# Optimization experiments

Hardware: AMD Instinct MI355X
Metric: run time of the kernel (lower is better)

Reference implementation:

```python
import jax, jax.numpy as jnp
import numpy as np


def dct_matrices(N):
    # torch_dct-style unnormalized DCT-II (norm=None): X_k = 2 * sum_n x_n cos(pi*(2n+1)k/(2N))
    n = jnp.arange(N, dtype=jnp.float32)
    ang = jnp.pi * (2.0 * n[None, :] + 1.0) * n[:, None] / (2.0 * N)  # [k, n]
    D = 2.0 * jnp.cos(ang)                                            # forward DCT matrix [k, n]
    w = jnp.where(n == 0, 0.5, 1.0)                                   # half-weight on DC term
    M = (jnp.cos(ang).T * w[None, :]) / (2.0 * N)                     # inverse DCT matrix [n, k]
    return D, M


def setup_inputs() -> dict:
    key = jax.random.key(0)
    k1, k2, k3 = jax.random.split(key, 3)
    B, c_in, c_out, H, W, kh, kw = 8, 64, 128, 128, 128, 5, 5
    K = float(np.sqrt(1.0 / (c_in * kh * kw)))
    x = jax.random.normal(k1, (B, c_in, H, W), dtype=jnp.float32)
    weight = (2.0 * jax.random.uniform(k2, (c_out, c_in, kh, kw), dtype=jnp.float32) - 1.0) * K
    bias = (2.0 * jax.random.uniform(k3, (c_out,), dtype=jnp.float32) - 1.0) * K
    return {"x": x, "weight": weight, "bias": bias}


def reference(x, weight, bias):
    B, c_in, H, W = x.shape
    c_out, _, kh, kw = weight.shape
    D, M = dct_matrices(H)

    # DCT-II along H axis of input
    xd = jnp.einsum('kh,bchw->bckw', D, x)            # (B, c_in, H, W)
    xf = jnp.fft.rfft(xd, axis=-1)                    # (B, c_in, H, Wf) complex

    # Pad kernel along H to full size, DCT along H, rFFT along W with n=W
    wpad = jnp.pad(weight, ((0, 0), (0, 0), (0, H - kh), (0, 0)))
    wd = jnp.einsum('kh,oihw->oikw', D, wpad)         # (c_out, c_in, H, kw)
    wf = jnp.fft.rfft(wd, n=W, axis=-1)               # (c_out, c_in, H, Wf) complex

    # Broadcast complex multiply + reduce over c_in (fused via einsum)
    hf = jnp.einsum('bchw,ochw->bohw', xf, wf)        # (B, c_out, H, Wf)
    h = jnp.fft.irfft(hf, n=W, axis=-1)               # (B, c_out, H, W)

    # Inverse DCT along H, add bias, stride slice (stride = 1)
    h = jnp.einsum('nk,bokw->bonw', M, h) + bias[None, :, None, None]
    return h[:, :, ::1, ::1]
```

## Files before the change

### kernel.cpp

```cpp
#include <hip/hip_runtime.h>


using half8v = __attribute__((ext_vector_type(8))) _Float16;
using half4v = __attribute__((ext_vector_type(4))) _Float16;
using f32x4  = __attribute__((ext_vector_type(4))) float;

#define PI_F 3.14159265358979323846f

__device__ __forceinline__ int sw_off(int n, int k, int K, int mask) {
    int c = k >> 3;
    return n * K + (((c ^ (n & mask)) << 3) | (k & 7));
}

__global__ void k_dm(_Float16* __restrict__ D, _Float16* __restrict__ M) {
    int k = blockIdx.x;
    int h = threadIdx.x;
    float ang = PI_F * (float)((2 * h + 1) * k) * (1.0f / 256.0f);
    float c = cosf(ang);
    D[k * 128 + h] = (_Float16)(2.0f * c);
    float wk = (k == 0) ? 0.5f : 1.0f;
    M[h * 128 + k] = (_Float16)(c * wk * (1.0f / 256.0f));
}

__global__ void k_wd(const float* __restrict__ w, _Float16* __restrict__ WD) {
    int bid = blockIdx.x;
    int kf = bid / 10, s = bid % 10;
    int j = s >> 1, ci0 = (s & 1) << 5;
    float dv[5];
#pragma unroll
    for (int i = 0; i < 5; ++i)
        dv[i] = 2.0f * cosf(PI_F * (float)((2 * i + 1) * kf) * (1.0f / 256.0f));
    for (int e = threadIdx.x; e < 4096; e += 256) {
        int co = e >> 5, t = e & 31, ci = ci0 + t;
        const float* wp = w + (co * 64 + ci) * 25 + j;
        float acc = 0.f;
#pragma unroll
        for (int i = 0; i < 5; ++i) acc += dv[i] * wp[i * 5];
        WD[bid * 4096 + e] = (_Float16)acc;
    }
}

__device__ __forceinline__ void gemm128(const _Float16* lA, const _Float16* lB,
                                        f32x4 acc[4][4], int tid) {
    int lane = tid & 63, ln = lane & 15, q = lane >> 4;
    int wave = tid >> 6, wm = wave >> 1, wn = wave & 1;
#pragma unroll
    for (int s = 0; s < 4; ++s) {
        half8v af[4], bf[4];
#pragma unroll
        for (int mt = 0; mt < 4; ++mt) {
            int m = wm * 64 + mt * 16 + ln;
            af[mt] = *(const half8v*)(&lA[m * 128 + (((s * 4 + q) ^ (m & 15)) << 3)]);
        }
#pragma unroll
        for (int nt = 0; nt < 4; ++nt) {
            int n = wn * 64 + nt * 16 + ln;
            bf[nt] = *(const half8v*)(&lB[n * 128 + (((s * 4 + q) ^ (n & 15)) << 3)]);
        }
#pragma unroll
        for (int mt = 0; mt < 4; ++mt)
#pragma unroll
            for (int nt = 0; nt < 4; ++nt)
                acc[mt][nt] = __builtin_amdgcn_mfma_f32_16x16x32_f16(af[mt], bf[nt], acc[mt][nt], 0, 0, 0);
    }
}

__device__ __forceinline__ void stage_copyA(const _Float16* __restrict__ g, _Float16* l, int tid) {
    const half8v* gs = (const half8v*)g;
#pragma unroll
    for (int r = 0; r < 8; ++r) {
        int gg = tid + r * 256;
        int m = gg >> 4, c = gg & 15;
        *(half8v*)(&l[m * 128 + (((c ^ (m & 15)) << 3))]) = gs[gg];
    }
}

__device__ __forceinline__ void stage_transB(const _Float16* __restrict__ src, int row_stride,
                                             _Float16* l, int K, int mask, int nblocks, int tid) {
    for (int blk = tid; blk < nblocks; blk += 256) {
        int kb = blk >> 4, wb = blk & 15;
        int k0 = kb * 4, w0 = wb * 8;
        half8v r0 = *(const half8v*)(&src[(k0 + 0) * row_stride + w0]);
        half8v r1 = *(const half8v*)(&src[(k0 + 1) * row_stride + w0]);
        half8v r2 = *(const half8v*)(&src[(k0 + 2) * row_stride + w0]);
        half8v r3 = *(const half8v*)(&src[(k0 + 3) * row_stride + w0]);
#pragma unroll
        for (int dw = 0; dw < 8; ++dw) {
            int n = w0 + dw;
            half4v p = {r0[dw], r1[dw], r2[dw], r3[dw]};
            *(half4v*)(&l[sw_off(n, k0, K, mask)]) = p;
        }
    }
}

__global__ __launch_bounds__(256) void k_dctH(const float* __restrict__ x,
                                              const _Float16* __restrict__ Dg,
                                              _Float16* __restrict__ xd) {
    __shared__ _Float16 lA[128 * 128];
    __shared__ _Float16 lB[128 * 128];
    int b = blockIdx.x >> 6, ci = blockIdx.x & 63;
    int tid = threadIdx.x;

    stage_copyA(Dg, lA, tid);

    const float* xs = x + (long)(b * 64 + ci) * 16384;
#pragma unroll
    for (int rep = 0; rep < 2; ++rep) {
        int blk = tid + rep * 256;
        int hb = blk >> 4, wb = blk & 15;
        int h0 = hb * 4, w0 = wb * 8;
        f32x4 f[4][2];
#pragma unroll
        for (int dh = 0; dh < 4; ++dh) {
            f[dh][0] = *(const f32x4*)(&xs[(h0 + dh) * 128 + w0]);
            f[dh][1] = *(const f32x4*)(&xs[(h0 + dh) * 128 + w0 + 4]);
        }
#pragma unroll
        for (int dw = 0; dw < 8; ++dw) {
            int n = w0 + dw;
            half4v p = {(_Float16)f[0][dw >> 2][dw & 3], (_Float16)f[1][dw >> 2][dw & 3],
                        (_Float16)f[2][dw >> 2][dw & 3], (_Float16)f[3][dw >> 2][dw & 3]};
            *(half4v*)(&lB[sw_off(n, h0, 128, 15)]) = p;
        }
    }
    __syncthreads();

    f32x4 acc[4][4] = {};
    gemm128(lA, lB, acc, tid);

    int lane = tid & 63, ln = lane & 15, q = lane >> 4;
    int wave = tid >> 6, wm = wave >> 1, wn = wave & 1;
#pragma unroll
    for (int mt = 0; mt < 4; ++mt)
#pragma unroll
        for (int nt = 0; nt < 4; ++nt)
#pragma unroll
            for (int r = 0; r < 4; ++r) {
                int kk = wm * 64 + mt * 16 + q * 4 + r;
                int wcol = wn * 64 + nt * 16 + ln;
                xd[((long)(kk * 8 + b) * 64 + ci) * 128 + wcol] = (_Float16)acc[mt][nt][r];
            }
}

__global__ __launch_bounds__(256) void k_conv(const _Float16* __restrict__ xd,
                                              const _Float16* __restrict__ WD,
                                              _Float16* __restrict__ y2) {
    __shared__ _Float16 lX[128 * 64];
    __shared__ _Float16 lW[2][128 * 40];
    int k = blockIdx.x >> 3, b = blockIdx.x & 7;
    int tid = threadIdx.x;

    const _Float16* xs = xd + (long)(k * 8 + b) * 8192;
    stage_transB(xs, 128, lX, 64, 7, 256, tid);

    {
        const half8v* wt0 = (const half8v*)(WD + (long)(k * 10) * 4096);
#pragma unroll
        for (int p = 0; p < 2; ++p) {
            int g = tid + p * 256;
            int m = g >> 2, c = g & 3;
            *(half8v*)(&lW[0][m * 40 + c * 8]) = wt0[g];
        }
    }
    __syncthreads();

    int lane = tid & 63, ln = lane & 15, q = lane >> 4;
    int wave = tid >> 6, wm = wave >> 1, wn = wave & 1;
    f32x4 acc[4][4] = {};

    for (int s = 0; s < 10; ++s) {
        half8v pf0, pf1;
        if (s < 9) {
            const half8v* wtn = (const half8v*)(WD + (long)(k * 10 + s + 1) * 4096);
            pf0 = wtn[tid];
            pf1 = wtn[tid + 256];
        }
        int j = s >> 1;
        int cb = (s & 1) << 2;
        const _Float16* lWc = lW[s & 1];
        half8v af[4], bf[4];
#pragma unroll
        for (int mt = 0; mt < 4; ++mt) {
            int m = wm * 64 + mt * 16 + ln;
            af[mt] = *(const half8v*)(&lWc[m * 40 + q * 8]);
        }
#pragma unroll
        for (int nt = 0; nt < 4; ++nt) {
            int wcol = wn * 64 + nt * 16 + ln;
            int n = (wcol - j) & 127;
            bf[nt] = *(const half8v*)(&lX[n * 64 + (((cb + q) ^ (n & 7)) << 3)]);
        }
#pragma unroll
        for (int mt = 0; mt < 4; ++mt)
#pragma unroll
            for (int nt = 0; nt < 4; ++nt)
                acc[mt][nt] = __builtin_amdgcn_mfma_f32_16x16x32_f16(af[mt], bf[nt], acc[mt][nt], 0, 0, 0);

        if (s < 9) {
            _Float16* dst = lW[(s + 1) & 1];
            {
                int g = tid;
                int m = g >> 2, c = g & 3;
                *(half8v*)(&dst[m * 40 + c * 8]) = pf0;
            }
            {
                int g = tid + 256;
                int m = g >> 2, c = g & 3;
                *(half8v*)(&dst[m * 40 + c * 8]) = pf1;
            }
            __syncthreads();
        }
    }

    _Float16* yb = y2 + (long)(b * 128 + k) * 16384;
#pragma unroll
    for (int mt = 0; mt < 4; ++mt)
#pragma unroll
        for (int nt = 0; nt < 4; ++nt)
#pragma unroll
            for (int r = 0; r < 4; ++r) {
                int co = wm * 64 + mt * 16 + q * 4 + r;
                int wcol = wn * 64 + nt * 16 + ln;
                yb[co * 128 + wcol] = (_Float16)acc[mt][nt][r];
            }
}

__global__ __launch_bounds__(256) void k_idct(const _Float16* __restrict__ y2,
                                              const _Float16* __restrict__ Mg,
                                              const float* __restrict__ bias,
                                              float* __restrict__ out) {
    __shared__ _Float16 lA[128 * 128];
    __shared__ _Float16 lB[128 * 128];
    int b = blockIdx.x >> 7, co = blockIdx.x & 127;
    int tid = threadIdx.x;

    stage_copyA(Mg, lA, tid);
    const _Float16* src = y2 + (long)b * 2097152 + co * 128;
    stage_transB(src, 16384, lB, 128, 15, 512, tid);
    __syncthreads();

    f32x4 acc[4][4] = {};
    gemm128(lA, lB, acc, tid);

    float bv = bias[co];
    float* ob = out + ((long)(b * 128 + co)) * 16384;
    int lane = tid & 63, ln = lane & 15, q = lane >> 4;
    int wave = tid >> 6, wm = wave >> 1, wn = wave & 1;
#pragma unroll
    for (int mt = 0; mt < 4; ++mt)
#pragma unroll
        for (int nt = 0; nt < 4; ++nt)
#pragma unroll
            for (int r = 0; r < 4; ++r) {
                int h = wm * 64 + mt * 16 + q * 4 + r;
                int wcol = wn * 64 + nt * 16 + ln;
                ob[h * 128 + wcol] = acc[mt][nt][r] + bv;
            }
}

extern "C" void kernel_launch(void* const* d_in, const int* in_sizes, int n_in,
                              void* d_out, int out_size, void* d_ws, size_t ws_size,
                              hipStream_t stream) {
    const float* x    = (const float*)d_in[0];
    const float* w    = (const float*)d_in[1];
    const float* bias = (const float*)d_in[2];
    float* out = (float*)d_out;

    char* ws = (char*)d_ws;
    _Float16* D  = (_Float16*)(ws);
    _Float16* M  = (_Float16*)(ws + 32768);
    _Float16* WD = (_Float16*)(ws + 65536);
    _Float16* xd = (_Float16*)(ws + 65536 + 10485760);
    _Float16* y2 = (_Float16*)(ws + 65536 + 10485760 + 16777216);

    k_dm  <<<dim3(128),  dim3(128), 0, stream>>>(D, M);
    k_wd  <<<dim3(1280), dim3(256), 0, stream>>>(w, WD);
    k_dctH<<<dim3(512),  dim3(256), 0, stream>>>(x, D, xd);
    k_conv<<<dim3(1024), dim3(256), 0, stream>>>(xd, WD, y2);
    k_idct<<<dim3(1024), dim3(256), 0, stream>>>(y2, M, bias, out);
}
```

Baseline: 160.6 us.

## Load conv weight fragments directly from global and reorder blocks by frequency

The conv kernel no longer stages the per-frequency weight tile through a double-buffered LDS array with per-step barriers. Each wave now reads its A fragments straight from global/L2, which removes nine __syncthreads and the LDS traffic. Block indexing also changes so that consecutive blocks share the same batch and cover different frequencies. The trade-off is that each weight tile is now fetched redundantly by multiple waves through cache, with unhidden global latency in the MFMA loop.

```diff
diff --git a/kernel.cpp b/kernel.cpp
--- a/kernel.cpp
+++ b/kernel.cpp
@@ -146,43 +146,29 @@
                                               const _Float16* __restrict__ WD,
                                               _Float16* __restrict__ y2) {
     __shared__ _Float16 lX[128 * 64];
-    __shared__ _Float16 lW[2][128 * 40];
-    int k = blockIdx.x >> 3, b = blockIdx.x & 7;
+    int bid = blockIdx.x;
+    int k = bid & 127, b = bid >> 7;
     int tid = threadIdx.x;
 
     const _Float16* xs = xd + (long)(k * 8 + b) * 8192;
     stage_transB(xs, 128, lX, 64, 7, 256, tid);
-
-    {
-        const half8v* wt0 = (const half8v*)(WD + (long)(k * 10) * 4096);
-#pragma unroll
-        for (int p = 0; p < 2; ++p) {
-            int g = tid + p * 256;
-            int m = g >> 2, c = g & 3;
-            *(half8v*)(&lW[0][m * 40 + c * 8]) = wt0[g];
-        }
-    }
     __syncthreads();
 
     int lane = tid & 63, ln = lane & 15, q = lane >> 4;
     int wave = tid >> 6, wm = wave >> 1, wn = wave & 1;
     f32x4 acc[4][4] = {};
 
+    const _Float16* wkb = WD + (long)k * 40960;
+
     for (int s = 0; s < 10; ++s) {
-        half8v pf0, pf1;
-        if (s < 9) {
-            const half8v* wtn = (const half8v*)(WD + (long)(k * 10 + s + 1) * 4096);
-            pf0 = wtn[tid];
-            pf1 = wtn[tid + 256];
-        }
         int j = s >> 1;
         int cb = (s & 1) << 2;
-        const _Float16* lWc = lW[s & 1];
+        const _Float16* wt = wkb + s * 4096;
         half8v af[4], bf[4];
 #pragma unroll
         for (int mt = 0; mt < 4; ++mt) {
             int m = wm * 64 + mt * 16 + ln;
-            af[mt] = *(const half8v*)(&lWc[m * 40 + q * 8]);
+            af[mt] = *(const half8v*)(&wt[m * 32 + q * 8]);
         }
 #pragma unroll
         for (int nt = 0; nt < 4; ++nt) {
@@ -195,21 +181,6 @@
 #pragma unroll
             for (int nt = 0; nt < 4; ++nt)
                 acc[mt][nt] = __builtin_amdgcn_mfma_f32_16x16x32_f16(af[mt], bf[nt], acc[mt][nt], 0, 0, 0);
-
-        if (s < 9) {
-            _Float16* dst = lW[(s + 1) & 1];
-            {
-                int g = tid;
-                int m = g >> 2, c = g & 3;
-                *(half8v*)(&dst[m * 40 + c * 8]) = pf0;
-            }
-            {
-                int g = tid + 256;
-                int m = g >> 2, c = g & 3;
-                *(half8v*)(&dst[m * 40 + c * 8]) = pf1;
-            }
-            __syncthreads();
-        }
     }
 
     _Float16* yb = y2 + (long)(b * 128 + k) * 16384;
```

After: 159.9 us. No clear change (-0.4%).
